# Kernel optimization log

Hardware: AMD Instinct MI355X
Metric: run time of the kernel (lower is better)

Reference implementation:

```python
import jax, jax.numpy as jnp
import numpy as np

N = 12000      # nodes
F = 128        # input feature dim
H = 32         # hidden_dim (hardcoded in module)
TOL = 1e-6     # tolerant_zero_error
AVG_DEG = 32.0


def _glorot(k, shape):
    lim = float(np.sqrt(6.0 / (shape[0] + shape[1])))
    return jax.random.uniform(k, shape, jnp.float32, -lim, lim)


def setup_inputs() -> dict:
    key = jax.random.key(0)
    ks = jax.random.split(key, 8)
    x = jax.random.normal(ks[0], (N, F), jnp.float32)
    # binary sparse-ish adjacency, ~32 neighbors/node, zero diagonal mostly
    a = (jax.random.uniform(ks[1], (N, N)) < (AVG_DEG / N)).astype(jnp.float32)
    W1 = _glorot(ks[2], (2 * F, H)); b1 = jnp.zeros((H,), jnp.float32)
    W2 = _glorot(ks[3], (2 * H, H)); b2 = jnp.zeros((H,), jnp.float32)
    W3 = _glorot(ks[4], (2 * H, H)); b3 = jnp.zeros((H,), jnp.float32)
    Wf1 = _glorot(ks[5], (H, 2 * H)); bf1 = jnp.zeros((2 * H,), jnp.float32)
    Wf2 = _glorot(ks[6], (2 * H, 1)); bf2 = jnp.zeros((1,), jnp.float32)
    return dict(x=x, a=a, W1=W1, b1=b1, W2=W2, b2=b2, W3=W3, b3=b3,
                Wf1=Wf1, bf1=bf1, Wf2=Wf2, bf2=bf2)


def reference(x, a, W1, b1, W2, b2, W3, b3, Wf1, bf1, Wf2, bf2):
    n = a.shape[0]
    idx = jnp.arange(n)
    # add_self_loop: +1 on diagonal entries that are (approximately) zero
    diag = jnp.diagonal(a)
    add = jnp.where(jnp.abs(diag) < TOL, 1.0, 0.0)
    a_hat = a.at[idx, idx].add(add)               # [N, N]
    deg = jnp.sum(a_hat, axis=1, keepdims=True)    # [N, 1], >= 1

    def sage_conv(h, W, b):
        agg = (a_hat @ h) / deg                    # mean neighbor aggregation
        o = jnp.concatenate([h, agg], axis=-1) @ W + b
        # tf.math.l2_normalize(axis=-1) semantics
        o = o / jnp.sqrt(jnp.maximum(jnp.sum(o * o, axis=-1, keepdims=True), 1e-12))
        return jnp.tanh(o)

    h = sage_conv(x, W1, b1)   # [N, 32]
    h = sage_conv(h, W2, b2)   # [N, 32]  (dropout skipped: training=False)
    h = sage_conv(h, W3, b3)   # [N, 32]
    p = jnp.sum(h, axis=0, keepdims=True)          # GlobalSumPool -> [1, 32]
    p = jnp.tanh(p @ Wf1 + bf1)                    # [1, 64]
    return p @ Wf2 + bf2                           # [1, 1]
```

## Files before the change

kernel.cpp:

```cpp
#include <hip/hip_runtime.h>

#define NN 12000
#define FF 128
#define HH 32
#define CAP 96
#define NBIN 64

typedef unsigned int uintv4 __attribute__((ext_vector_type(4)));

__global__ __launch_bounds__(256) void k_scan(const float* __restrict__ a,
                                              unsigned short* __restrict__ adj,
                                              int* __restrict__ deg,
                                              float* __restrict__ partial) {
  const int row = blockIdx.x, tid = threadIdx.x;
  __shared__ int cnt;
  __shared__ unsigned short slist[CAP];
  if (tid == 0) cnt = 0;
  if (row == 0) {
    for (int i = tid; i < NBIN * HH; i += 256) partial[i] = 0.f;
  }
  __syncthreads();

  const uintv4* arow = (const uintv4*)(a + (size_t)row * NN);
  uintv4 v[12];
  #pragma unroll
  for (int i = 0; i < 12; ++i) {
    const int c = tid + i * 256;
    uintv4 z = {0u, 0u, 0u, 0u};
    v[i] = (c < NN / 4) ? arow[c] : z;
  }
  #pragma unroll
  for (int i = 0; i < 12; ++i) {
    const int c = tid + i * 256;
    uintv4 w = v[i];
    if ((w.x | w.y | w.z | w.w) == 0u) continue;
    int j0 = 4 * c;
    if (w.x && j0     != row) { int p = atomicAdd(&cnt, 1); if (p < CAP-1) slist[p] = (unsigned short)(j0    ); }
    if (w.y && j0 + 1 != row) { int p = atomicAdd(&cnt, 1); if (p < CAP-1) slist[p] = (unsigned short)(j0 + 1); }
    if (w.z && j0 + 2 != row) { int p = atomicAdd(&cnt, 1); if (p < CAP-1) slist[p] = (unsigned short)(j0 + 2); }
    if (w.w && j0 + 3 != row) { int p = atomicAdd(&cnt, 1); if (p < CAP-1) slist[p] = (unsigned short)(j0 + 3); }
  }
  __syncthreads();
  const int c = min(cnt, CAP - 1);
  if (tid == 0) { slist[c] = (unsigned short)row; deg[row] = c + 1; }
  __syncthreads();
  if (tid < c + 1) adj[(size_t)row * CAP + tid] = slist[tid];
}

__global__ __launch_bounds__(256) void k_xw1(const float* __restrict__ x,
    const float* __restrict__ W ,
    float* __restrict__ Z, float* __restrict__ Y) {
  __shared__ float sW[FF * 64];
  __shared__ float sx[4][FF];
  const int tid = threadIdx.x;
  for (int i = tid; i < FF * 64; i += 256) {
    int f = i >> 6, k = i & 63;
    sW[i] = (k < HH) ? W[f * HH + k] : W[(FF + f) * HH + (k - HH)];
  }
  const int wave = tid >> 6, lane = tid & 63;
  const int node = blockIdx.x * 4 + wave;
  float2 xi = *(const float2*)(x + (size_t)node * FF + lane * 2);
  __syncthreads();
  sx[wave][2 * lane] = xi.x;
  sx[wave][2 * lane + 1] = xi.y;
  __syncthreads();

  float acc = 0.f;
  const float* xr = sx[wave];
  #pragma unroll 8
  for (int f = 0; f < FF; ++f) acc += xr[f] * sW[f * 64 + lane];
  if (lane < HH) Z[(size_t)node * HH + lane] = acc;
  else           Y[(size_t)node * HH + (lane - HH)] = acc;
}

__global__ __launch_bounds__(256) void k_gl1(const float* __restrict__ Z,
    const float* __restrict__ Y, const float* __restrict__ b,
    const unsigned short* __restrict__ adj, const int* __restrict__ deg,
    float* __restrict__ hout) {
  __shared__ unsigned short sidx[4][CAP];
  const int tid = threadIdx.x;
  const int wave = tid >> 6, lane = tid & 63;
  const int k = lane & 31, g = lane >> 5;
  const int node = blockIdx.x * 4 + wave;
  const int d = deg[node];
  for (int n = lane; n < d; n += 64)
    sidx[wave][n] = adj[(size_t)node * CAP + n];
  __syncthreads();

  float p0 = 0.f, p1 = 0.f, p2 = 0.f, p3 = 0.f;
  int n = g;
  for (; n + 6 < d; n += 8) {
    p0 += Y[(size_t)sidx[wave][n    ] * HH + k];
    p1 += Y[(size_t)sidx[wave][n + 2] * HH + k];
    p2 += Y[(size_t)sidx[wave][n + 4] * HH + k];
    p3 += Y[(size_t)sidx[wave][n + 6] * HH + k];
  }
  for (; n < d; n += 2)
    p0 += Y[(size_t)sidx[wave][n] * HH + k];
  float agg = (p0 + p1) + (p2 + p3);
  agg += __shfl_xor(agg, 32);
  agg *= 1.0f / (float)d;
  float o = Z[(size_t)node * HH + k] + agg + b[k];
  float ss = o * o;
  for (int off = 16; off; off >>= 1) ss += __shfl_xor(ss, off, 32);
  float r = rsqrtf(fmaxf(ss, 1e-12f));
  if (lane < 32) hout[(size_t)node * HH + k] = tanhf(o * r);
}

__global__ __launch_bounds__(256) void k_sageh(const float* __restrict__ hin,
    const float* __restrict__ W , const float* __restrict__ b,
    const unsigned short* __restrict__ adj, const int* __restrict__ deg,
    float* __restrict__ hout) {
  __shared__ float sW[2 * HH * HH];
  __shared__ float sb[HH];
  __shared__ float sbuf[4][2 * HH];
  __shared__ unsigned short sidx[4][CAP];
  const int tid = threadIdx.x;
  for (int i = tid; i < 2 * HH * HH; i += 256) sW[i] = W[i];
  if (tid < HH) sb[tid] = b[tid];

  const int wave = tid >> 6, lane = tid & 63;
  const int k = lane & 31, g = lane >> 5;
  const int node = blockIdx.x * 4 + wave;
  const int d = deg[node];
  for (int n = lane; n < d; n += 64)
    sidx[wave][n] = adj[(size_t)node * CAP + n];
  __syncthreads();

  float p0 = 0.f, p1 = 0.f, p2 = 0.f, p3 = 0.f;
  int n = g;
  for (; n + 6 < d; n += 8) {
    p0 += hin[(size_t)sidx[wave][n    ] * HH + k];
    p1 += hin[(size_t)sidx[wave][n + 2] * HH + k];
    p2 += hin[(size_t)sidx[wave][n + 4] * HH + k];
    p3 += hin[(size_t)sidx[wave][n + 6] * HH + k];
  }
  for (; n < d; n += 2)
    p0 += hin[(size_t)sidx[wave][n] * HH + k];
  float agg = (p0 + p1) + (p2 + p3);
  agg += __shfl_xor(agg, 32);
  agg *= 1.0f / (float)d;
  float hi = hin[(size_t)node * HH + k];
  if (g == 0) { sbuf[wave][k] = hi; sbuf[wave][HH + k] = agg; }
  __syncthreads();

  float acc = 0.f;
  const float* bufh = sbuf[wave];
  const int f0 = g * 16;
  #pragma unroll
  for (int f = f0; f < f0 + 16; ++f) {
    acc += bufh[f]      * sW[f * HH + k];
    acc += bufh[HH + f] * sW[(HH + f) * HH + k];
  }
  acc += __shfl_xor(acc, 32);
  acc += sb[k];
  float ss = acc * acc;
  for (int off = 16; off; off >>= 1) ss += __shfl_xor(ss, off, 32);
  float r = rsqrtf(fmaxf(ss, 1e-12f));
  if (lane < 32) hout[(size_t)node * HH + k] = tanhf(acc * r);
}

__global__ __launch_bounds__(256) void k_sageh3(const float* __restrict__ hin,
    const float* __restrict__ W, const float* __restrict__ b,
    const unsigned short* __restrict__ adj, const int* __restrict__ deg,
    float* __restrict__ partial) {
  __shared__ float sW[2 * HH * HH];
  __shared__ float sb[HH];
  __shared__ float sbuf[4][2 * HH];
  __shared__ float red[4][HH];
  __shared__ unsigned short sidx[4][CAP];
  const int tid = threadIdx.x;
  for (int i = tid; i < 2 * HH * HH; i += 256) sW[i] = W[i];
  if (tid < HH) sb[tid] = b[tid];

  const int wave = tid >> 6, lane = tid & 63;
  const int k = lane & 31, g = lane >> 5;
  const int node = blockIdx.x * 4 + wave;
  const int d = deg[node];
  for (int n = lane; n < d; n += 64)
    sidx[wave][n] = adj[(size_t)node * CAP + n];
  __syncthreads();

  float p0 = 0.f, p1 = 0.f, p2 = 0.f, p3 = 0.f;
  int n = g;
  for (; n + 6 < d; n += 8) {
    p0 += hin[(size_t)sidx[wave][n    ] * HH + k];
    p1 += hin[(size_t)sidx[wave][n + 2] * HH + k];
    p2 += hin[(size_t)sidx[wave][n + 4] * HH + k];
    p3 += hin[(size_t)sidx[wave][n + 6] * HH + k];
  }
  for (; n < d; n += 2)
    p0 += hin[(size_t)sidx[wave][n] * HH + k];
  float agg = (p0 + p1) + (p2 + p3);
  agg += __shfl_xor(agg, 32);
  agg *= 1.0f / (float)d;
  float hi = hin[(size_t)node * HH + k];
  if (g == 0) { sbuf[wave][k] = hi; sbuf[wave][HH + k] = agg; }
  __syncthreads();

  float acc = 0.f;
  const float* bufh = sbuf[wave];
  const int f0 = g * 16;
  #pragma unroll
  for (int f = f0; f < f0 + 16; ++f) {
    acc += bufh[f]      * sW[f * HH + k];
    acc += bufh[HH + f] * sW[(HH + f) * HH + k];
  }
  acc += __shfl_xor(acc, 32);
  acc += sb[k];
  float ss = acc * acc;
  for (int off = 16; off; off >>= 1) ss += __shfl_xor(ss, off, 32);
  float r = rsqrtf(fmaxf(ss, 1e-12f));
  if (lane < 32) red[wave][k] = tanhf(acc * r);
  __syncthreads();
  if (tid < HH) {
    float t = (red[0][tid] + red[1][tid]) + (red[2][tid] + red[3][tid]);
    atomicAdd(&partial[(blockIdx.x & (NBIN - 1)) * HH + tid], t);
  }
}

__global__ __launch_bounds__(64) void k_final(const float* __restrict__ partial,
    const float* __restrict__ Wf1, const float* __restrict__ bf1,
    const float* __restrict__ Wf2, const float* __restrict__ bf2,
    float* __restrict__ out) {
  __shared__ float sp[HH];
  const int lane = threadIdx.x;
  if (lane < HH) {
    float s = 0.f;
    for (int bb = 0; bb < NBIN; ++bb) s += partial[bb * HH + lane];
    sp[lane] = s;
  }
  __syncthreads();
  float q = bf1[lane];
  for (int f = 0; f < HH; ++f) q += sp[f] * Wf1[f * 64 + lane];
  q = tanhf(q);
  float rsum = q * Wf2[lane];
  for (int off = 32; off; off >>= 1) rsum += __shfl_xor(rsum, off);
  if (lane == 0) out[0] = rsum + bf2[0];
}

extern "C" void kernel_launch(void* const* d_in, const int* in_sizes, int n_in,
                              void* d_out, int out_size, void* d_ws, size_t ws_size,
                              hipStream_t stream) {
  const float* x   = (const float*)d_in[0];
  const float* a   = (const float*)d_in[1];
  const float* W1  = (const float*)d_in[2];
  const float* b1  = (const float*)d_in[3];
  const float* W2  = (const float*)d_in[4];
  const float* b2  = (const float*)d_in[5];
  const float* W3  = (const float*)d_in[6];
  const float* b3  = (const float*)d_in[7];
  const float* Wf1 = (const float*)d_in[8];
  const float* bf1 = (const float*)d_in[9];
  const float* Wf2 = (const float*)d_in[10];
  const float* bf2 = (const float*)d_in[11];

  char* ws = (char*)d_ws;
  unsigned short* adj = (unsigned short*)ws;  ws += (size_t)NN * CAP * sizeof(unsigned short);
  int*   deg     = (int*)ws;                  ws += (size_t)((NN * sizeof(int) + 255) & ~(size_t)255);
  float* Zb      = (float*)ws;                ws += (size_t)NN * HH * sizeof(float);
  float* Yb      = (float*)ws;                ws += (size_t)NN * HH * sizeof(float);
  float* h1      = (float*)ws;                ws += (size_t)NN * HH * sizeof(float);
  float* h2      = (float*)ws;                ws += (size_t)NN * HH * sizeof(float);
  float* partial = (float*)ws;

  hipLaunchKernelGGL(k_scan,   dim3(NN),     dim3(256), 0, stream, a, adj, deg, partial);
  hipLaunchKernelGGL(k_xw1,    dim3(NN / 4), dim3(256), 0, stream, x, W1, Zb, Yb);
  hipLaunchKernelGGL(k_gl1,    dim3(NN / 4), dim3(256), 0, stream, Zb, Yb, b1, adj, deg, h1);
  hipLaunchKernelGGL(k_sageh,  dim3(NN / 4), dim3(256), 0, stream, h1, W2, b2, adj, deg, h2);
  hipLaunchKernelGGL(k_sageh3, dim3(NN / 4), dim3(256), 0, stream, h2, W3, b3, adj, deg, partial);
  hipLaunchKernelGGL(k_final,  dim3(1),      dim3(64),  0, stream, partial, Wf1, bf1, Wf2, bf2, (float*)d_out);
}
```

Baseline: 161.1 us.

## Fuse x·W1 projection into adjacency scan and final MLP into last layer

Folds the first-layer feature projection into the adjacency-scan kernel, so each row block also computes its node's Z/Y outputs from W1 read through global memory. The final pooling MLP moves into the last SAGE kernel through a last-block-done atomic counter. Together these remove two kernel launches and the separate pass over x. In exchange, W1 is reread uncached per row and the scan kernel carries extra work and shared memory.

```diff
diff --git a/kernel.cpp b/kernel.cpp
--- a/kernel.cpp
+++ b/kernel.cpp
@@ -5,20 +5,26 @@
 #define HH 32
 #define CAP 96
 #define NBIN 64
+#define NB4 (NN / 4)
 
 typedef unsigned int uintv4 __attribute__((ext_vector_type(4)));
 
 __global__ __launch_bounds__(256) void k_scan(const float* __restrict__ a,
-                                              unsigned short* __restrict__ adj,
-                                              int* __restrict__ deg,
-                                              float* __restrict__ partial) {
+    const float* __restrict__ x, const float* __restrict__ W1,
+    unsigned short* __restrict__ adj, int* __restrict__ deg,
+    float* __restrict__ Z, float* __restrict__ Y,
+    float* __restrict__ partial, int* __restrict__ done) {
   const int row = blockIdx.x, tid = threadIdx.x;
   __shared__ int cnt;
   __shared__ unsigned short slist[CAP];
+  __shared__ float sx[FF];
+  __shared__ float sacc[4][64];
   if (tid == 0) cnt = 0;
   if (row == 0) {
     for (int i = tid; i < NBIN * HH; i += 256) partial[i] = 0.f;
-  }
+    if (tid == 0) *done = 0;
+  }
+  if (tid < FF) sx[tid] = x[(size_t)row * FF + tid];
   __syncthreads();
 
   const uintv4* arow = (const uintv4*)(a + (size_t)row * NN);
@@ -45,32 +51,25 @@
   if (tid == 0) { slist[c] = (unsigned short)row; deg[row] = c + 1; }
   __syncthreads();
   if (tid < c + 1) adj[(size_t)row * CAP + tid] = slist[tid];
-}
-
-__global__ __launch_bounds__(256) void k_xw1(const float* __restrict__ x,
-    const float* __restrict__ W ,
-    float* __restrict__ Z, float* __restrict__ Y) {
-  __shared__ float sW[FF * 64];
-  __shared__ float sx[4][FF];
-  const int tid = threadIdx.x;
-  for (int i = tid; i < FF * 64; i += 256) {
-    int f = i >> 6, k = i & 63;
-    sW[i] = (k < HH) ? W[f * HH + k] : W[(FF + f) * HH + (k - HH)];
-  }
-  const int wave = tid >> 6, lane = tid & 63;
-  const int node = blockIdx.x * 4 + wave;
-  float2 xi = *(const float2*)(x + (size_t)node * FF + lane * 2);
-  __syncthreads();
-  sx[wave][2 * lane] = xi.x;
-  sx[wave][2 * lane + 1] = xi.y;
-  __syncthreads();
-
-  float acc = 0.f;
-  const float* xr = sx[wave];
-  #pragma unroll 8
-  for (int f = 0; f < FF; ++f) acc += xr[f] * sW[f * 64 + lane];
-  if (lane < HH) Z[(size_t)node * HH + lane] = acc;
-  else           Y[(size_t)node * HH + (lane - HH)] = acc;
+
+  {
+    const int j = tid & 31;
+    const int half = (tid >> 5) & 1;
+    const int ch = tid >> 6;
+    const float* Wb = W1 + (size_t)(half * FF) * HH;
+    float acc = 0.f;
+    const int f0 = ch * 32;
+    #pragma unroll 8
+    for (int f = f0; f < f0 + 32; ++f)
+      acc += sx[f] * Wb[f * HH + j];
+    sacc[ch][tid & 63] = acc;
+  }
+  __syncthreads();
+  if (tid < 64) {
+    float o = (sacc[0][tid] + sacc[1][tid]) + (sacc[2][tid] + sacc[3][tid]);
+    if (tid < HH) Z[(size_t)row * HH + tid] = o;
+    else          Y[(size_t)row * HH + (tid - HH)] = o;
+  }
 }
 
 __global__ __launch_bounds__(256) void k_gl1(const float* __restrict__ Z,
@@ -163,12 +162,18 @@
 __global__ __launch_bounds__(256) void k_sageh3(const float* __restrict__ hin,
     const float* __restrict__ W, const float* __restrict__ b,
     const unsigned short* __restrict__ adj, const int* __restrict__ deg,
-    float* __restrict__ partial) {
+    float* __restrict__ partial, int* __restrict__ done,
+    const float* __restrict__ Wf1, const float* __restrict__ bf1,
+    const float* __restrict__ Wf2, const float* __restrict__ bf2,
+    float* __restrict__ out) {
   __shared__ float sW[2 * HH * HH];
   __shared__ float sb[HH];
   __shared__ float sbuf[4][2 * HH];
   __shared__ float red[4][HH];
   __shared__ unsigned short sidx[4][CAP];
+  __shared__ float sred[8][HH];
+  __shared__ float sp[HH];
+  __shared__ int amLast;
   const int tid = threadIdx.x;
   for (int i = tid; i < 2 * HH * HH; i += 256) sW[i] = W[i];
   if (tid < HH) sb[tid] = b[tid];
@@ -217,26 +222,40 @@
     float t = (red[0][tid] + red[1][tid]) + (red[2][tid] + red[3][tid]);
     atomicAdd(&partial[(blockIdx.x & (NBIN - 1)) * HH + tid], t);
   }
-}
-
-__global__ __launch_bounds__(64) void k_final(const float* __restrict__ partial,
-    const float* __restrict__ Wf1, const float* __restrict__ bf1,
-    const float* __restrict__ Wf2, const float* __restrict__ bf2,
-    float* __restrict__ out) {
-  __shared__ float sp[HH];
-  const int lane = threadIdx.x;
-  if (lane < HH) {
+  __syncthreads();
+  if (tid == 0) {
+    __threadfence();
+    amLast = (atomicAdd(done, 1) == NB4 - 1) ? 1 : 0;
+  }
+  __syncthreads();
+  if (!amLast) return;
+
+  __threadfence();
+  {
+    const int col = tid & 31, ch = tid >> 5;
     float s = 0.f;
-    for (int bb = 0; bb < NBIN; ++bb) s += partial[bb * HH + lane];
-    sp[lane] = s;
-  }
-  __syncthreads();
-  float q = bf1[lane];
-  for (int f = 0; f < HH; ++f) q += sp[f] * Wf1[f * 64 + lane];
-  q = tanhf(q);
-  float rsum = q * Wf2[lane];
-  for (int off = 32; off; off >>= 1) rsum += __shfl_xor(rsum, off);
-  if (lane == 0) out[0] = rsum + bf2[0];
+    for (int bb = ch; bb < NBIN; bb += 8)
+      s += __hip_atomic_load(&partial[bb * HH + col], __ATOMIC_RELAXED,
+                             __HIP_MEMORY_SCOPE_AGENT);
+    sred[ch][col] = s;
+  }
+  __syncthreads();
+  if (tid < HH) {
+    float t = 0.f;
+    #pragma unroll
+    for (int c2 = 0; c2 < 8; ++c2) t += sred[c2][tid];
+    sp[tid] = t;
+  }
+  __syncthreads();
+  if (tid < 64) {
+    float q = bf1[tid];
+    #pragma unroll
+    for (int f = 0; f < HH; ++f) q += sp[f] * Wf1[f * 64 + tid];
+    q = tanhf(q);
+    float rs = q * Wf2[tid];
+    for (int off = 32; off; off >>= 1) rs += __shfl_xor(rs, off);
+    if (tid == 0) out[0] = rs + bf2[0];
+  }
 }
 
 extern "C" void kernel_launch(void* const* d_in, const int* in_sizes, int n_in,
@@ -262,12 +281,13 @@
   float* Yb      = (float*)ws;                ws += (size_t)NN * HH * sizeof(float);
   float* h1      = (float*)ws;                ws += (size_t)NN * HH * sizeof(float);
   float* h2      = (float*)ws;                ws += (size_t)NN * HH * sizeof(float);
-  float* partial = (float*)ws;
-
-  hipLaunchKernelGGL(k_scan,   dim3(NN),     dim3(256), 0, stream, a, adj, deg, partial);
-  hipLaunchKernelGGL(k_xw1,    dim3(NN / 4), dim3(256), 0, stream, x, W1, Zb, Yb);
-  hipLaunchKernelGGL(k_gl1,    dim3(NN / 4), dim3(256), 0, stream, Zb, Yb, b1, adj, deg, h1);
-  hipLaunchKernelGGL(k_sageh,  dim3(NN / 4), dim3(256), 0, stream, h1, W2, b2, adj, deg, h2);
-  hipLaunchKernelGGL(k_sageh3, dim3(NN / 4), dim3(256), 0, stream, h2, W3, b3, adj, deg, partial);
-  hipLaunchKernelGGL(k_final,  dim3(1),      dim3(64),  0, stream, partial, Wf1, bf1, Wf2, bf2, (float*)d_out);
-}
+  float* partial = (float*)ws;                ws += (size_t)NBIN * HH * sizeof(float);
+  int*   done    = (int*)ws;
+
+  hipLaunchKernelGGL(k_scan,   dim3(NN),  dim3(256), 0, stream,
+                     a, x, W1, adj, deg, Zb, Yb, partial, done);
+  hipLaunchKernelGGL(k_gl1,    dim3(NB4), dim3(256), 0, stream, Zb, Yb, b1, adj, deg, h1);
+  hipLaunchKernelGGL(k_sageh,  dim3(NB4), dim3(256), 0, stream, h1, W2, b2, adj, deg, h2);
+  hipLaunchKernelGGL(k_sageh3, dim3(NB4), dim3(256), 0, stream,
+                     h2, W3, b3, adj, deg, partial, done, Wf1, bf1, Wf2, bf2, (float*)d_out);
+}
```

After: 192.9 us. 19.8% more time.

## Fuse three SAGE layers and final MLP into one persistent kernel with grid barriers

Applied to the files above, without the earlier changes.

Replaces the k_gl1, k_sageh, k_sageh3 and k_final launches with one persistent kernel of 1280 blocks. Each wave handles up to three nodes per layer, and a software grid barrier (atomic counter plus generation flag) separates the layers. The final MLP runs in the last block to finish, detected through an atomic ticket, so the separate single-block launch goes away. The goal is to remove launch gaps and tail effects between the small kernels. The cost is barrier spin latency, and the kernel can deadlock if all 1280 blocks cannot be co-resident (the code relies on launch_bounds with 6 blocks per CU).

```diff
diff --git a/kernel.cpp b/kernel.cpp
--- a/kernel.cpp
+++ b/kernel.cpp
@@ -5,19 +5,43 @@
 #define HH 32
 #define CAP 96
 #define NBIN 64
+#define NB4 (NN / 4)
+#define NBT 1280
+#define NWT (NBT * 4)
+#define ITMAX 3
 
 typedef unsigned int uintv4 __attribute__((ext_vector_type(4)));
+
+__device__ __forceinline__ void gridbar(int* __restrict__ bar) {
+  __syncthreads();
+  if (threadIdx.x == 0) {
+    __threadfence();
+    int g = __hip_atomic_load(&bar[1], __ATOMIC_RELAXED, __HIP_MEMORY_SCOPE_AGENT);
+    int old = __hip_atomic_fetch_add(&bar[0], 1, __ATOMIC_RELAXED, __HIP_MEMORY_SCOPE_AGENT);
+    if (old == NBT - 1) {
+      __hip_atomic_store(&bar[0], 0, __ATOMIC_RELAXED, __HIP_MEMORY_SCOPE_AGENT);
+      __hip_atomic_store(&bar[1], g + 1, __ATOMIC_RELEASE, __HIP_MEMORY_SCOPE_AGENT);
+    } else {
+      while (__hip_atomic_load(&bar[1], __ATOMIC_RELAXED, __HIP_MEMORY_SCOPE_AGENT) == g)
+        __builtin_amdgcn_s_sleep(4);
+    }
+    __threadfence();
+  }
+  __syncthreads();
+}
 
 __global__ __launch_bounds__(256) void k_scan(const float* __restrict__ a,
                                               unsigned short* __restrict__ adj,
                                               int* __restrict__ deg,
-                                              float* __restrict__ partial) {
+                                              float* __restrict__ partial,
+                                              int* __restrict__ ctrl) {
   const int row = blockIdx.x, tid = threadIdx.x;
   __shared__ int cnt;
   __shared__ unsigned short slist[CAP];
   if (tid == 0) cnt = 0;
   if (row == 0) {
     for (int i = tid; i < NBIN * HH; i += 256) partial[i] = 0.f;
+    if (tid < 4) ctrl[tid] = 0;
   }
   __syncthreads();
 
@@ -73,170 +97,206 @@
   else           Y[(size_t)node * HH + (lane - HH)] = acc;
 }
 
-__global__ __launch_bounds__(256) void k_gl1(const float* __restrict__ Z,
-    const float* __restrict__ Y, const float* __restrict__ b,
+__global__ __launch_bounds__(256, 6) void k_tail(
+    const float* __restrict__ Z, const float* __restrict__ Y,
+    const float* __restrict__ b1,
+    const float* __restrict__ W2, const float* __restrict__ b2,
+    const float* __restrict__ W3, const float* __restrict__ b3,
+    const float* __restrict__ Wf1, const float* __restrict__ bf1,
+    const float* __restrict__ Wf2, const float* __restrict__ bf2,
     const unsigned short* __restrict__ adj, const int* __restrict__ deg,
-    float* __restrict__ hout) {
-  __shared__ unsigned short sidx[4][CAP];
-  const int tid = threadIdx.x;
-  const int wave = tid >> 6, lane = tid & 63;
-  const int k = lane & 31, g = lane >> 5;
-  const int node = blockIdx.x * 4 + wave;
-  const int d = deg[node];
-  for (int n = lane; n < d; n += 64)
-    sidx[wave][n] = adj[(size_t)node * CAP + n];
-  __syncthreads();
-
-  float p0 = 0.f, p1 = 0.f, p2 = 0.f, p3 = 0.f;
-  int n = g;
-  for (; n + 6 < d; n += 8) {
-    p0 += Y[(size_t)sidx[wave][n    ] * HH + k];
-    p1 += Y[(size_t)sidx[wave][n + 2] * HH + k];
-    p2 += Y[(size_t)sidx[wave][n + 4] * HH + k];
-    p3 += Y[(size_t)sidx[wave][n + 6] * HH + k];
-  }
-  for (; n < d; n += 2)
-    p0 += Y[(size_t)sidx[wave][n] * HH + k];
-  float agg = (p0 + p1) + (p2 + p3);
-  agg += __shfl_xor(agg, 32);
-  agg *= 1.0f / (float)d;
-  float o = Z[(size_t)node * HH + k] + agg + b[k];
-  float ss = o * o;
-  for (int off = 16; off; off >>= 1) ss += __shfl_xor(ss, off, 32);
-  float r = rsqrtf(fmaxf(ss, 1e-12f));
-  if (lane < 32) hout[(size_t)node * HH + k] = tanhf(o * r);
-}
-
-__global__ __launch_bounds__(256) void k_sageh(const float* __restrict__ hin,
-    const float* __restrict__ W , const float* __restrict__ b,
-    const unsigned short* __restrict__ adj, const int* __restrict__ deg,
-    float* __restrict__ hout) {
+    float* __restrict__ h1, float* __restrict__ h2,
+    float* __restrict__ partial, int* __restrict__ ctrl,
+    float* __restrict__ out) {
   __shared__ float sW[2 * HH * HH];
   __shared__ float sb[HH];
   __shared__ float sbuf[4][2 * HH];
   __shared__ unsigned short sidx[4][CAP];
-  const int tid = threadIdx.x;
-  for (int i = tid; i < 2 * HH * HH; i += 256) sW[i] = W[i];
-  if (tid < HH) sb[tid] = b[tid];
-
+  __shared__ float red[8][HH];
+  __shared__ float sp[HH];
+  __shared__ int amLast;
+
+  const int tid = threadIdx.x, bid = blockIdx.x;
   const int wave = tid >> 6, lane = tid & 63;
   const int k = lane & 31, g = lane >> 5;
-  const int node = blockIdx.x * 4 + wave;
-  const int d = deg[node];
-  for (int n = lane; n < d; n += 64)
-    sidx[wave][n] = adj[(size_t)node * CAP + n];
-  __syncthreads();
-
-  float p0 = 0.f, p1 = 0.f, p2 = 0.f, p3 = 0.f;
-  int n = g;
-  for (; n + 6 < d; n += 8) {
-    p0 += hin[(size_t)sidx[wave][n    ] * HH + k];
-    p1 += hin[(size_t)sidx[wave][n + 2] * HH + k];
-    p2 += hin[(size_t)sidx[wave][n + 4] * HH + k];
-    p3 += hin[(size_t)sidx[wave][n + 6] * HH + k];
-  }
-  for (; n < d; n += 2)
-    p0 += hin[(size_t)sidx[wave][n] * HH + k];
-  float agg = (p0 + p1) + (p2 + p3);
-  agg += __shfl_xor(agg, 32);
-  agg *= 1.0f / (float)d;
-  float hi = hin[(size_t)node * HH + k];
-  if (g == 0) { sbuf[wave][k] = hi; sbuf[wave][HH + k] = agg; }
-  __syncthreads();
-
-  float acc = 0.f;
-  const float* bufh = sbuf[wave];
-  const int f0 = g * 16;
-  #pragma unroll
-  for (int f = f0; f < f0 + 16; ++f) {
-    acc += bufh[f]      * sW[f * HH + k];
-    acc += bufh[HH + f] * sW[(HH + f) * HH + k];
-  }
-  acc += __shfl_xor(acc, 32);
-  acc += sb[k];
-  float ss = acc * acc;
-  for (int off = 16; off; off >>= 1) ss += __shfl_xor(ss, off, 32);
-  float r = rsqrtf(fmaxf(ss, 1e-12f));
-  if (lane < 32) hout[(size_t)node * HH + k] = tanhf(acc * r);
-}
-
-__global__ __launch_bounds__(256) void k_sageh3(const float* __restrict__ hin,
-    const float* __restrict__ W, const float* __restrict__ b,
-    const unsigned short* __restrict__ adj, const int* __restrict__ deg,
-    float* __restrict__ partial) {
-  __shared__ float sW[2 * HH * HH];
-  __shared__ float sb[HH];
-  __shared__ float sbuf[4][2 * HH];
-  __shared__ float red[4][HH];
-  __shared__ unsigned short sidx[4][CAP];
-  const int tid = threadIdx.x;
-  for (int i = tid; i < 2 * HH * HH; i += 256) sW[i] = W[i];
-  if (tid < HH) sb[tid] = b[tid];
-
-  const int wave = tid >> 6, lane = tid & 63;
-  const int k = lane & 31, g = lane >> 5;
-  const int node = blockIdx.x * 4 + wave;
-  const int d = deg[node];
-  for (int n = lane; n < d; n += 64)
-    sidx[wave][n] = adj[(size_t)node * CAP + n];
-  __syncthreads();
-
-  float p0 = 0.f, p1 = 0.f, p2 = 0.f, p3 = 0.f;
-  int n = g;
-  for (; n + 6 < d; n += 8) {
-    p0 += hin[(size_t)sidx[wave][n    ] * HH + k];
-    p1 += hin[(size_t)sidx[wave][n + 2] * HH + k];
-    p2 += hin[(size_t)sidx[wave][n + 4] * HH + k];
-    p3 += hin[(size_t)sidx[wave][n + 6] * HH + k];
-  }
-  for (; n < d; n += 2)
-    p0 += hin[(size_t)sidx[wave][n] * HH + k];
-  float agg = (p0 + p1) + (p2 + p3);
-  agg += __shfl_xor(agg, 32);
-  agg *= 1.0f / (float)d;
-  float hi = hin[(size_t)node * HH + k];
-  if (g == 0) { sbuf[wave][k] = hi; sbuf[wave][HH + k] = agg; }
-  __syncthreads();
-
-  float acc = 0.f;
-  const float* bufh = sbuf[wave];
-  const int f0 = g * 16;
-  #pragma unroll
-  for (int f = f0; f < f0 + 16; ++f) {
-    acc += bufh[f]      * sW[f * HH + k];
-    acc += bufh[HH + f] * sW[(HH + f) * HH + k];
-  }
-  acc += __shfl_xor(acc, 32);
-  acc += sb[k];
-  float ss = acc * acc;
-  for (int off = 16; off; off >>= 1) ss += __shfl_xor(ss, off, 32);
-  float r = rsqrtf(fmaxf(ss, 1e-12f));
-  if (lane < 32) red[wave][k] = tanhf(acc * r);
+  const int wid = bid * 4 + wave;
+  int* bar = ctrl + 1;
+
+  for (int it = 0; it < ITMAX; ++it) {
+    const int node = wid + it * NWT;
+    const bool act = node < NN;
+    int d = 0;
+    if (act) {
+      d = deg[node];
+      for (int n = lane; n < d; n += 64)
+        sidx[wave][n] = adj[(size_t)node * CAP + n];
+    }
+    __syncthreads();
+    if (act) {
+      float p0 = 0.f, p1 = 0.f, p2 = 0.f, p3 = 0.f;
+      int n = g;
+      for (; n + 6 < d; n += 8) {
+        p0 += Y[(size_t)sidx[wave][n    ] * HH + k];
+        p1 += Y[(size_t)sidx[wave][n + 2] * HH + k];
+        p2 += Y[(size_t)sidx[wave][n + 4] * HH + k];
+        p3 += Y[(size_t)sidx[wave][n + 6] * HH + k];
+      }
+      for (; n < d; n += 2)
+        p0 += Y[(size_t)sidx[wave][n] * HH + k];
+      float agg = (p0 + p1) + (p2 + p3);
+      agg += __shfl_xor(agg, 32);
+      agg *= 1.0f / (float)d;
+      float o = Z[(size_t)node * HH + k] + agg + b1[k];
+      float ss = o * o;
+      for (int off = 16; off; off >>= 1) ss += __shfl_xor(ss, off, 32);
+      float r = rsqrtf(fmaxf(ss, 1e-12f));
+      if (lane < 32) h1[(size_t)node * HH + k] = tanhf(o * r);
+    }
+    __syncthreads();
+  }
+  gridbar(bar);
+
+  for (int i = tid; i < 2 * HH * HH; i += 256) sW[i] = W2[i];
+  if (tid < HH) sb[tid] = b2[tid];
+  __syncthreads();
+  for (int it = 0; it < ITMAX; ++it) {
+    const int node = wid + it * NWT;
+    const bool act = node < NN;
+    int d = 0;
+    if (act) {
+      d = deg[node];
+      for (int n = lane; n < d; n += 64)
+        sidx[wave][n] = adj[(size_t)node * CAP + n];
+    }
+    __syncthreads();
+    if (act) {
+      float p0 = 0.f, p1 = 0.f, p2 = 0.f, p3 = 0.f;
+      int n = g;
+      for (; n + 6 < d; n += 8) {
+        p0 += h1[(size_t)sidx[wave][n    ] * HH + k];
+        p1 += h1[(size_t)sidx[wave][n + 2] * HH + k];
+        p2 += h1[(size_t)sidx[wave][n + 4] * HH + k];
+        p3 += h1[(size_t)sidx[wave][n + 6] * HH + k];
+      }
+      for (; n < d; n += 2)
+        p0 += h1[(size_t)sidx[wave][n] * HH + k];
+      float agg = (p0 + p1) + (p2 + p3);
+      agg += __shfl_xor(agg, 32);
+      agg *= 1.0f / (float)d;
+      float hi = h1[(size_t)node * HH + k];
+      if (g == 0) { sbuf[wave][k] = hi; sbuf[wave][HH + k] = agg; }
+    }
+    __syncthreads();
+    if (act) {
+      float acc = 0.f;
+      const float* bufh = sbuf[wave];
+      const int f0 = g * 16;
+      #pragma unroll
+      for (int f = f0; f < f0 + 16; ++f) {
+        acc += bufh[f]      * sW[f * HH + k];
+        acc += bufh[HH + f] * sW[(HH + f) * HH + k];
+      }
+      acc += __shfl_xor(acc, 32);
+      acc += sb[k];
+      float ss = acc * acc;
+      for (int off = 16; off; off >>= 1) ss += __shfl_xor(ss, off, 32);
+      float r = rsqrtf(fmaxf(ss, 1e-12f));
+      if (lane < 32) h2[(size_t)node * HH + k] = tanhf(acc * r);
+    }
+    __syncthreads();
+  }
+  gridbar(bar);
+
+  for (int i = tid; i < 2 * HH * HH; i += 256) sW[i] = W3[i];
+  if (tid < HH) sb[tid] = b3[tid];
+  __syncthreads();
+  float pacc = 0.f;
+  for (int it = 0; it < ITMAX; ++it) {
+    const int node = wid + it * NWT;
+    const bool act = node < NN;
+    int d = 0;
+    if (act) {
+      d = deg[node];
+      for (int n = lane; n < d; n += 64)
+        sidx[wave][n] = adj[(size_t)node * CAP + n];
+    }
+    __syncthreads();
+    if (act) {
+      float p0 = 0.f, p1 = 0.f, p2 = 0.f, p3 = 0.f;
+      int n = g;
+      for (; n + 6 < d; n += 8) {
+        p0 += h2[(size_t)sidx[wave][n    ] * HH + k];
+        p1 += h2[(size_t)sidx[wave][n + 2] * HH + k];
+        p2 += h2[(size_t)sidx[wave][n + 4] * HH + k];
+        p3 += h2[(size_t)sidx[wave][n + 6] * HH + k];
+      }
+      for (; n < d; n += 2)
+        p0 += h2[(size_t)sidx[wave][n] * HH + k];
+      float agg = (p0 + p1) + (p2 + p3);
+      agg += __shfl_xor(agg, 32);
+      agg *= 1.0f / (float)d;
+      float hi = h2[(size_t)node * HH + k];
+      if (g == 0) { sbuf[wave][k] = hi; sbuf[wave][HH + k] = agg; }
+    }
+    __syncthreads();
+    if (act) {
+      float acc = 0.f;
+      const float* bufh = sbuf[wave];
+      const int f0 = g * 16;
+      #pragma unroll
+      for (int f = f0; f < f0 + 16; ++f) {
+        acc += bufh[f]      * sW[f * HH + k];
+        acc += bufh[HH + f] * sW[(HH + f) * HH + k];
+      }
+      acc += __shfl_xor(acc, 32);
+      acc += sb[k];
+      float ss = acc * acc;
+      for (int off = 16; off; off >>= 1) ss += __shfl_xor(ss, off, 32);
+      float r = rsqrtf(fmaxf(ss, 1e-12f));
+      if (lane < 32) pacc += tanhf(acc * r);
+    }
+    __syncthreads();
+  }
+  if (lane < 32) red[wave][k] = pacc;
   __syncthreads();
   if (tid < HH) {
     float t = (red[0][tid] + red[1][tid]) + (red[2][tid] + red[3][tid]);
-    atomicAdd(&partial[(blockIdx.x & (NBIN - 1)) * HH + tid], t);
-  }
-}
-
-__global__ __launch_bounds__(64) void k_final(const float* __restrict__ partial,
-    const float* __restrict__ Wf1, const float* __restrict__ bf1,
-    const float* __restrict__ Wf2, const float* __restrict__ bf2,
-    float* __restrict__ out) {
-  __shared__ float sp[HH];
-  const int lane = threadIdx.x;
-  if (lane < HH) {
+    atomicAdd(&partial[(bid & (NBIN - 1)) * HH + tid], t);
+  }
+  __syncthreads();
+  if (tid == 0) {
+    __threadfence();
+    amLast = (atomicAdd(&ctrl[0], 1) == NBT - 1) ? 1 : 0;
+  }
+  __syncthreads();
+  if (!amLast) return;
+
+  __threadfence();
+  {
+    const int col = tid & 31, ch = tid >> 5;
     float s = 0.f;
-    for (int bb = 0; bb < NBIN; ++bb) s += partial[bb * HH + lane];
-    sp[lane] = s;
-  }
-  __syncthreads();
-  float q = bf1[lane];
-  for (int f = 0; f < HH; ++f) q += sp[f] * Wf1[f * 64 + lane];
-  q = tanhf(q);
-  float rsum = q * Wf2[lane];
-  for (int off = 32; off; off >>= 1) rsum += __shfl_xor(rsum, off);
-  if (lane == 0) out[0] = rsum + bf2[0];
+    for (int bb = ch; bb < NBIN; bb += 8)
+      s += __hip_atomic_load(&partial[bb * HH + col], __ATOMIC_RELAXED,
+                             __HIP_MEMORY_SCOPE_AGENT);
+    red[ch][col] = s;
+  }
+  __syncthreads();
+  if (tid < HH) {
+    float t = 0.f;
+    #pragma unroll
+    for (int c2 = 0; c2 < 8; ++c2) t += red[c2][tid];
+    sp[tid] = t;
+  }
+  __syncthreads();
+  if (tid < 64) {
+    float q = bf1[tid];
+    #pragma unroll
+    for (int f = 0; f < HH; ++f) q += sp[f] * Wf1[f * 64 + tid];
+    q = tanhf(q);
+    float rs = q * Wf2[tid];
+    for (int off = 32; off; off >>= 1) rs += __shfl_xor(rs, off);
+    if (tid == 0) out[0] = rs + bf2[0];
+  }
 }
 
 extern "C" void kernel_launch(void* const* d_in, const int* in_sizes, int n_in,
@@ -262,12 +322,12 @@
   float* Yb      = (float*)ws;                ws += (size_t)NN * HH * sizeof(float);
   float* h1      = (float*)ws;                ws += (size_t)NN * HH * sizeof(float);
   float* h2      = (float*)ws;                ws += (size_t)NN * HH * sizeof(float);
-  float* partial = (float*)ws;
-
-  hipLaunchKernelGGL(k_scan,   dim3(NN),     dim3(256), 0, stream, a, adj, deg, partial);
-  hipLaunchKernelGGL(k_xw1,    dim3(NN / 4), dim3(256), 0, stream, x, W1, Zb, Yb);
-  hipLaunchKernelGGL(k_gl1,    dim3(NN / 4), dim3(256), 0, stream, Zb, Yb, b1, adj, deg, h1);
-  hipLaunchKernelGGL(k_sageh,  dim3(NN / 4), dim3(256), 0, stream, h1, W2, b2, adj, deg, h2);
-  hipLaunchKernelGGL(k_sageh3, dim3(NN / 4), dim3(256), 0, stream, h2, W3, b3, adj, deg, partial);
-  hipLaunchKernelGGL(k_final,  dim3(1),      dim3(64),  0, stream, partial, Wf1, bf1, Wf2, bf2, (float*)d_out);
-}
+  float* partial = (float*)ws;                ws += (size_t)NBIN * HH * sizeof(float);
+  int*   ctrl    = (int*)ws;
+
+  hipLaunchKernelGGL(k_scan, dim3(NN),  dim3(256), 0, stream, a, adj, deg, partial, ctrl);
+  hipLaunchKernelGGL(k_xw1,  dim3(NB4), dim3(256), 0, stream, x, W1, Zb, Yb);
+  hipLaunchKernelGGL(k_tail, dim3(NBT), dim3(256), 0, stream,
+                     Zb, Yb, b1, W2, b2, W3, b3, Wf1, bf1, Wf2, bf2,
+                     adj, deg, h1, h2, partial, ctrl, (float*)d_out);
+}
```

After: 480.4 us. +198.3%, slower.
